# Kernel optimization log

Hardware: AMD Instinct MI355X
Metric: run time of the kernel (lower is better)

Reference implementation:

```python
import jax, jax.numpy as jnp
import numpy as np

N_CONCEPTS = 32
D_MODEL = 512
COMMITMENT_COST = 0.25


def setup_inputs() -> dict:
    key = jax.random.key(0)
    kx, kc = jax.random.split(key)
    x = jax.random.normal(kx, (8, 8192, D_MODEL), dtype=jnp.float32)
    codebook = jax.random.normal(kc, (N_CONCEPTS, D_MODEL), dtype=jnp.float32) * 0.02
    return {"x": x, "codebook": codebook}


def reference(x, codebook):
    B, T, D = x.shape
    x_flat = x.reshape(B * T, D)
    x2 = jnp.sum(x_flat * x_flat, axis=1, keepdims=True)          # [BT,1]
    c2 = jnp.sum(codebook * codebook, axis=1)                      # [K]
    xc = jnp.einsum('nd,kd->nk', x_flat, codebook)                 # [BT,K]
    dists = x2 + c2 - 2.0 * xc
    nearest_idx = jnp.argmin(dists, axis=1)                        # [BT]
    q = codebook[nearest_idx]                                      # gather [BT,D]
    # straight-through estimator
    quantized = x_flat + jax.lax.stop_gradient(q - x_flat)
    vq_loss = (jnp.mean((jax.lax.stop_gradient(quantized) - x_flat) ** 2)
               + COMMITMENT_COST * jnp.mean((quantized - jax.lax.stop_gradient(x_flat)) ** 2))
    # histogram of concept usage (fused replacement of the per-concept loop)
    counts = jnp.zeros((N_CONCEPTS,), dtype=jnp.int32).at[nearest_idx].add(1)
    return quantized.reshape(B, T, D), vq_loss, counts
```

## Files before the change

kernel.cpp:

```cpp
#include <hip/hip_runtime.h>

#define BT_ROWS 65536
#define DIM     512
#define NK      32
#define TPB     128
#define RPB     64
#define NBLK    (BT_ROWS / RPB)
#define CHUNK   64
#define NCHUNK  (DIM / CHUNK)

typedef float f4 __attribute__((ext_vector_type(4)));
typedef float f32x16 __attribute__((ext_vector_type(16)));
typedef short bf16x8 __attribute__((ext_vector_type(8)));
typedef unsigned int u32x4 __attribute__((ext_vector_type(4)));
typedef const __attribute__((address_space(1))) void GAS;
typedef __attribute__((address_space(3))) void LAS;

union Frag { u32x4 q; unsigned int w[4]; bf16x8 v; };


__global__ void vq_prep(const float* __restrict__ cb, float* __restrict__ c2,
                        int* __restrict__ counts, unsigned int* __restrict__ cbh32) {
    int t = threadIdx.x;
    const f4* c4 = (const f4*)cb;
#pragma unroll
    for (int i = 0; i < 16; ++i) {
        f4 v = c4[t * 16 + i];
        unsigned int w0, w1;
        asm("v_cvt_pk_bf16_f32 %0, %1, %2" : "=v"(w0) : "v"(v.x), "v"(v.y));
        asm("v_cvt_pk_bf16_f32 %0, %1, %2" : "=v"(w1) : "v"(v.z), "v"(v.w));
        cbh32[t * 32 + 2 * i]     = w0;
        cbh32[t * 32 + 2 * i + 1] = w1;
    }
    if (t < NK) {
        float s = 0.f;
#pragma unroll 8
        for (int i = 0; i < DIM / 4; ++i) {
            f4 v = c4[t * (DIM / 4) + i];
            s += v.x * v.x + v.y * v.y + v.z * v.z + v.w * v.w;
        }
        c2[t] = s;
    } else if (t < 2 * NK) {
        counts[t - NK] = 0;
    }
}

__global__ __launch_bounds__(TPB, 4) void vq_main(const float* __restrict__ x,
                                                  const float* __restrict__ cb,
                                                  const float* __restrict__ c2,
                                                  const unsigned short* __restrict__ cbh,
                                                  float* __restrict__ out,
                                                  float* __restrict__ blockloss,
                                                  int* __restrict__ counts) {
    const int tid  = threadIdx.x;
    const int lane = tid & 63;
    const int wv   = tid >> 6;
    const int tb   = wv * 32;
    const int R0   = blockIdx.x * RPB;

    __shared__ float         xbuf[2][RPB][CHUNK];
    __shared__ float         bestd[RPB];
    __shared__ float         x2row[RPB];
    __shared__ unsigned char karr[RPB];
    __shared__ int           hist[NK];
    if (tid < NK) hist[tid] = 0;

    const char* stsrc[8];
#pragma unroll
    for (int t = 0; t < 8; ++t) {
        int rl = wv * 32 + t * 4 + (lane >> 4);
        int g  = (lane & 15) ^ (rl & 15);
        stsrc[t] = (const char*)x + (size_t)(R0 + rl) * (DIM * 4) + g * 16;
    }
#define STAGE(b, c) do {                                                         \
    _Pragma("unroll")                                                            \
    for (int t = 0; t < 8; ++t)                                                  \
        __builtin_amdgcn_global_load_lds((GAS*)(stsrc[t] + (size_t)(c) * 256),   \
                                         (LAS*)&xbuf[b][wv * 32 + t * 4][0],     \
                                         16, 0, 0);                              \
} while (0)

    f32x16 acc;
#pragma unroll
    for (int r = 0; r < 16; ++r) acc[r] = 0.f;
    float x2acc = 0.f;

    const int m   = tb + (lane & 31);
    const int sw  = m & 15;
    const int n   = lane & 31;
    const int kh  = (lane >> 5) << 3;
    const float c2v = c2[n];

    STAGE(0, 0);
    asm volatile("s_waitcnt vmcnt(0)" ::: "memory");
    __syncthreads();

#pragma unroll 1
    for (int c = 0; c < NCHUNK; ++c) {
        const int cur = c & 1;
        if (c + 1 < NCHUNK) STAGE(cur ^ 1, c + 1);

        const f4* xrow = (const f4*)&xbuf[cur][m][0];
#pragma unroll
        for (int s = 0; s < 4; ++s) {
            const int tg = s * 4 + ((lane >> 5) << 1);
            f4 a0 = xrow[tg ^ sw];
            f4 a1 = xrow[(tg + 1) ^ sw];
            x2acc += a0.x * a0.x + a0.y * a0.y + a0.z * a0.z + a0.w * a0.w
                   + a1.x * a1.x + a1.y * a1.y + a1.z * a1.z + a1.w * a1.w;

            Frag fa;
            asm("v_cvt_pk_bf16_f32 %0, %1, %2" : "=v"(fa.w[0]) : "v"(a0.x), "v"(a0.y));
            asm("v_cvt_pk_bf16_f32 %0, %1, %2" : "=v"(fa.w[1]) : "v"(a0.z), "v"(a0.w));
            asm("v_cvt_pk_bf16_f32 %0, %1, %2" : "=v"(fa.w[2]) : "v"(a1.x), "v"(a1.y));
            asm("v_cvt_pk_bf16_f32 %0, %1, %2" : "=v"(fa.w[3]) : "v"(a1.z), "v"(a1.w));

            Frag fb;
            fb.q = *(const u32x4*)(cbh + (size_t)n * DIM + c * CHUNK + s * 16 + kh);

            acc = __builtin_amdgcn_mfma_f32_32x32x16_bf16(fa.v, fb.v, acc, 0, 0, 0);
        }
        asm volatile("s_waitcnt vmcnt(0)" ::: "memory");
        __syncthreads();
    }
#undef STAGE

    {
        float o = __shfl_xor(x2acc, 32, 64);
        if (lane < 32) x2row[tb + lane] = x2acc + o;
    }

#pragma unroll
    for (int r = 0; r < 16; ++r) {
        float val = c2v - 2.f * acc[r];
        int   idx = n;
#pragma unroll
        for (int off = 1; off <= 16; off <<= 1) {
            float ov = __shfl_xor(val, off, 64);
            int   oi = __shfl_xor(idx, off, 64);
            if (ov < val || (ov == val && oi < idx)) { val = ov; idx = oi; }
        }
        const int mrow = tb + (r & 3) + 8 * (r >> 2) + ((lane >> 5) << 2);
        if ((lane & 31) == 0) { bestd[mrow] = val; karr[mrow] = (unsigned char)idx; }
    }
    __syncthreads();

    if (tid < RPB) {
        float ls = x2row[tid] + bestd[tid];
        atomicAdd(&hist[karr[tid]], 1);
#pragma unroll
        for (int mo = 32; mo; mo >>= 1) ls += __shfl_xor(ls, mo, 64);
        if (tid == 0) blockloss[blockIdx.x] = ls;
    }
    __syncthreads();
    if (tid < NK) {
        int h = hist[tid];
        if (h) atomicAdd(&counts[tid], h);
    }

    const f4* __restrict__ cb4 = (const f4*)cb;
    f4* __restrict__ o4 = (f4*)out;
#pragma unroll 1
    for (int rr = 0; rr < 32; ++rr) {
        int    kr   = karr[tb + rr];
        size_t base = (size_t)(R0 + tb + rr) * (DIM / 4);
        o4[base + lane]      = cb4[kr * (DIM / 4) + lane];
        o4[base + 64 + lane] = cb4[kr * (DIM / 4) + 64 + lane];
    }
}

__global__ void vq_final(const float* __restrict__ blockloss, const int* __restrict__ counts,
                         float* __restrict__ out) {
    int   t = threadIdx.x;
    float v = blockloss[t] + blockloss[t + 256] + blockloss[t + 512] + blockloss[t + 768];
#pragma unroll
    for (int m = 32; m; m >>= 1) v += __shfl_xor(v, m, 64);
    __shared__ float red[4];
    if ((t & 63) == 0) red[t >> 6] = v;
    __syncthreads();
    if (t == 0)
        out[(size_t)BT_ROWS * DIM] =
            1.25f * (red[0] + red[1] + red[2] + red[3]) / (float)((size_t)BT_ROWS * DIM);
    if (t < NK)
        out[(size_t)BT_ROWS * DIM + 1 + t] = (float)counts[t];
}

extern "C" void kernel_launch(void* const* d_in, const int* in_sizes, int n_in,
                              void* d_out, int out_size, void* d_ws, size_t ws_size,
                              hipStream_t stream) {
    const float* x  = (const float*)d_in[0];
    const float* cb = (const float*)d_in[1];
    float* out = (float*)d_out;

    float* f         = (float*)d_ws;
    float* c2        = f;
    float* blockloss = f + NK;
    int*   counts    = (int*)(f + NK + NBLK);
    unsigned int*   cbh32 = (unsigned int*)((char*)d_ws + 8192);
    unsigned short* cbh   = (unsigned short*)cbh32;

    vq_prep<<<1, 256, 0, stream>>>(cb, c2, counts, cbh32);
    vq_main<<<NBLK, TPB, 0, stream>>>(x, cb, c2, cbh, out, blockloss, counts);
    vq_final<<<1, 256, 0, stream>>>(blockloss, counts, out);
}
```

Baseline: 70.59 us.

## Replace LDS-direct loads with register-staged triple-buffered prefetch, drop block barriers

The global_load_lds staging is replaced by a software pipeline. Each thread loads its x tiles into registers three chunks ahead, then writes them to a double-buffered LDS region with a new XOR swizzle. Each wave now stages and consumes only its own 32 rows, so the per-chunk s_waitcnt and __syncthreads are removed and the chunk loop is fully unrolled. Chunk width drops to 32 floats and launch bounds are relaxed to 2 blocks per CU. This gives more registers for the prefetch buffers, at the risk of lower occupancy and higher VGPR pressure.

```diff
diff --git a/kernel.cpp b/kernel.cpp
--- a/kernel.cpp
+++ b/kernel.cpp
@@ -6,15 +6,13 @@
 #define TPB     128
 #define RPB     64
 #define NBLK    (BT_ROWS / RPB)
-#define CHUNK   64
+#define CHUNK   32
 #define NCHUNK  (DIM / CHUNK)
 
 typedef float f4 __attribute__((ext_vector_type(4)));
 typedef float f32x16 __attribute__((ext_vector_type(16)));
 typedef short bf16x8 __attribute__((ext_vector_type(8)));
 typedef unsigned int u32x4 __attribute__((ext_vector_type(4)));
-typedef const __attribute__((address_space(1))) void GAS;
-typedef __attribute__((address_space(3))) void LAS;
 
 union Frag { u32x4 q; unsigned int w[4]; bf16x8 v; };
 
@@ -45,7 +43,7 @@
     }
 }
 
-__global__ __launch_bounds__(TPB, 4) void vq_main(const float* __restrict__ x,
+__global__ __launch_bounds__(TPB, 2) void vq_main(const float* __restrict__ x,
                                                   const float* __restrict__ cb,
                                                   const float* __restrict__ c2,
                                                   const unsigned short* __restrict__ cbh,
@@ -65,19 +63,26 @@
     __shared__ int           hist[NK];
     if (tid < NK) hist[tid] = 0;
 
-    const char* stsrc[8];
-#pragma unroll
-    for (int t = 0; t < 8; ++t) {
-        int rl = wv * 32 + t * 4 + (lane >> 4);
-        int g  = (lane & 15) ^ (rl & 15);
-        stsrc[t] = (const char*)x + (size_t)(R0 + rl) * (DIM * 4) + g * 16;
-    }
-#define STAGE(b, c) do {                                                         \
+    const char* xsrc[4];
+    int         ldsoff[4];
+#pragma unroll
+    for (int t = 0; t < 4; ++t) {
+        int rl    = tb + t * 8 + (lane >> 3);
+        xsrc[t]   = (const char*)x + (size_t)(R0 + rl) * (DIM * 4) + (lane & 7) * 16;
+        ldsoff[t] = rl * CHUNK + (((lane & 7) ^ (lane >> 3)) << 2);
+    }
+    float* const lds0 = &xbuf[0][0][0];
+
+    f4 rs[3][4];
+#define GLOAD(c) do {                                                            \
     _Pragma("unroll")                                                            \
-    for (int t = 0; t < 8; ++t)                                                  \
-        __builtin_amdgcn_global_load_lds((GAS*)(stsrc[t] + (size_t)(c) * 256),   \
-                                         (LAS*)&xbuf[b][wv * 32 + t * 4][0],     \
-                                         16, 0, 0);                              \
+    for (int t = 0; t < 4; ++t)                                                  \
+        rs[(c) % 3][t] = *(const f4*)(xsrc[t] + (size_t)(c) * 128);              \
+} while (0)
+#define DSWRITE(c) do {                                                          \
+    _Pragma("unroll")                                                            \
+    for (int t = 0; t < 4; ++t)                                                  \
+        *(f4*)(lds0 + (((c) & 1) * (RPB * CHUNK)) + ldsoff[t]) = rs[(c) % 3][t]; \
 } while (0)
 
     f32x16 acc;
@@ -86,23 +91,22 @@
     float x2acc = 0.f;
 
     const int m   = tb + (lane & 31);
-    const int sw  = m & 15;
+    const int sw  = m & 7;
     const int n   = lane & 31;
     const int kh  = (lane >> 5) << 3;
     const float c2v = c2[n];
 
-    STAGE(0, 0);
-    asm volatile("s_waitcnt vmcnt(0)" ::: "memory");
-    __syncthreads();
-
-#pragma unroll 1
+    GLOAD(0); GLOAD(1); GLOAD(2);
+    DSWRITE(0);
+
+#pragma unroll
     for (int c = 0; c < NCHUNK; ++c) {
-        const int cur = c & 1;
-        if (c + 1 < NCHUNK) STAGE(cur ^ 1, c + 1);
-
-        const f4* xrow = (const f4*)&xbuf[cur][m][0];
-#pragma unroll
-        for (int s = 0; s < 4; ++s) {
+        if (c + 3 < NCHUNK) GLOAD(c + 3);
+        if (c + 1 < NCHUNK) DSWRITE(c + 1);
+
+        const f4* xrow = (const f4*)&xbuf[c & 1][m][0];
+#pragma unroll
+        for (int s = 0; s < 2; ++s) {
             const int tg = s * 4 + ((lane >> 5) << 1);
             f4 a0 = xrow[tg ^ sw];
             f4 a1 = xrow[(tg + 1) ^ sw];
@@ -120,10 +124,9 @@
 
             acc = __builtin_amdgcn_mfma_f32_32x32x16_bf16(fa.v, fb.v, acc, 0, 0, 0);
         }
-        asm volatile("s_waitcnt vmcnt(0)" ::: "memory");
-        __syncthreads();
-    }
-#undef STAGE
+    }
+#undef GLOAD
+#undef DSWRITE
 
     {
         float o = __shfl_xor(x2acc, 32, 64);
```

Measured after the change: 72.50 us. 1.03x slower.
